# Optimization experiments

Measured on AMD Instinct MI355X. Metric: run time of the kernel, lower is better.

Reference implementation:

```python
import jax, jax.numpy as jnp
import numpy as np
import math

N_LAYER, N_EMBD, LAYER_ID = 12, 768, 0
B, T, C = 32, 1024, N_EMBD


def _init_params():
    r01 = LAYER_ID / (N_LAYER - 1)          # ratio_0_to_1
    r1a0 = 1.0 - LAYER_ID / N_LAYER          # ratio_1_to_almost0
    h = np.arange(C, dtype=np.float32)
    time_decay = (-5.0 + 8.0 * (h / (C - 1)) ** (0.7 + 1.3 * r01)).astype(np.float32)
    zigzag = (np.array([(i + 1) % 3 - 1 for i in range(C)], dtype=np.float32)) * 0.5
    time_first = (np.ones(C, dtype=np.float32) * math.log(0.3) + zigzag).astype(np.float32)
    xlin = (np.arange(C, dtype=np.float32) / C).reshape(1, 1, C)
    time_mix_k = np.power(xlin, r1a0).astype(np.float32)
    time_mix_v = (np.power(xlin, r1a0) + 0.3 * r01).astype(np.float32)
    time_mix_r = np.power(xlin, 0.5 * r1a0).astype(np.float32)
    return time_decay, time_first, time_mix_k, time_mix_v, time_mix_r


def setup_inputs() -> dict:
    key = jax.random.key(0)
    ks = jax.random.split(key, 5)
    td, tf, tmk, tmv, tmr = _init_params()
    scale = 0.02
    return {
        'x': jax.random.normal(ks[0], (B, T, C), dtype=jnp.float32),
        'time_decay': jnp.asarray(td),
        'time_first': jnp.asarray(tf),
        'time_mix_k': jnp.asarray(tmk),
        'time_mix_v': jnp.asarray(tmv),
        'time_mix_r': jnp.asarray(tmr),
        'Wk': jax.random.normal(ks[1], (C, C), dtype=jnp.float32) * scale,
        'Wv': jax.random.normal(ks[2], (C, C), dtype=jnp.float32) * scale,
        'Wr': jax.random.normal(ks[3], (C, C), dtype=jnp.float32) * scale,
        'Wo': jax.random.normal(ks[4], (C, C), dtype=jnp.float32) * scale,
    }


def _wkv(w, u, k, v):
    # Numerically-stable WKV recurrence (Vision-RWKV kernel math):
    # y_t = (sum_{i<t} exp(w*(t-1-i)+k_i) v_i + exp(u+k_t) v_t) / (same denom)
    # carry: p = num*exp(-o), q = den*exp(-o), o = running log-scale; shapes [B,C]
    def step(carry, kv):
        p, q, o = carry
        kt, vt = kv  # [B,C]
        no = jnp.maximum(o, u + kt)
        A = jnp.exp(o - no)
        Bc = jnp.exp(u + kt - no)
        y = (A * p + Bc * vt) / (A * q + Bc)
        no2 = jnp.maximum(w + o, kt)
        A2 = jnp.exp(w + o - no2)
        B2 = jnp.exp(kt - no2)
        return (A2 * p + B2 * vt, A2 * q + B2, no2), y

    b = k.shape[0]
    init = (jnp.zeros((b, C), jnp.float32), jnp.zeros((b, C), jnp.float32),
            jnp.full((b, C), -1e38, jnp.float32))
    kT = jnp.swapaxes(k, 0, 1)  # [T,B,C]
    vT = jnp.swapaxes(v, 0, 1)
    _, ys = jax.lax.scan(step, init, (kT, vT))
    return jnp.swapaxes(ys, 0, 1)  # [B,T,C]


def reference(x, time_decay, time_first, time_mix_k, time_mix_v, time_mix_r, Wk, Wv, Wr, Wo):
    # time_shift: xx[t] = x[t-1], xx[0] = 0
    xx = jnp.pad(x, ((0, 0), (1, 0), (0, 0)))[:, :-1, :]
    xk = x * time_mix_k + xx * (1.0 - time_mix_k)
    xv = x * time_mix_v + xx * (1.0 - time_mix_v)
    xr = x * time_mix_r + xx * (1.0 - time_mix_r)
    k = jnp.einsum('btc,oc->bto', xk, Wk)
    v = jnp.einsum('btc,oc->bto', xv, Wv)
    r = jnp.einsum('btc,oc->bto', xr, Wr)
    sr = jax.nn.sigmoid(r)
    y = _wkv(time_decay, time_first, k, v)
    return jnp.einsum('btc,oc->bto', sr * y, Wo)
```

## Files before the change

kernel.cpp:

```cpp
#include <hip/hip_runtime.h>
#include <math.h>

#define B_ 32
#define T_ 1024
#define C_ 768
#define M_ (B_ * T_)

typedef __attribute__((ext_vector_type(8))) short bf16x8;
typedef __attribute__((ext_vector_type(4))) float f32x4;
typedef __attribute__((ext_vector_type(8))) unsigned short u16x8;
typedef __attribute__((address_space(1))) const void g_void;
typedef __attribute__((address_space(3))) void lds_void;

__device__ __forceinline__ unsigned short f2bf(float f) {
  union { float f; unsigned int u; } v; v.f = f;
  unsigned int u = v.u;
  u += 0x7fffu + ((u >> 16) & 1u);
  return (unsigned short)(u >> 16);
}
__device__ __forceinline__ float b2f(unsigned short h) {
  union { unsigned int u; float f; } v; v.u = ((unsigned int)h) << 16;
  return v.f;
}
__device__ __forceinline__ float blo(unsigned int p) {
  union { unsigned int u; float f; } v; v.u = p << 16;
  return v.f;
}
__device__ __forceinline__ float bhi(unsigned int p) {
  union { unsigned int u; float f; } v; v.u = p & 0xffff0000u;
  return v.f;
}

#define WPB 288
#define WBLK (4 * WPB)
#define MBLK ((M_ * C_ / 8) / 256)

__global__ __launch_bounds__(256) void prep(const float* __restrict__ x,
                                            const float* __restrict__ tmk,
                                            const float* __restrict__ tmv,
                                            const float* __restrict__ tmr,
                                            const float* __restrict__ Wk,
                                            const float* __restrict__ Wv,
                                            const float* __restrict__ Wr,
                                            const float* __restrict__ Wo,
                                            unsigned short* __restrict__ wbk,
                                            unsigned short* __restrict__ wbv,
                                            unsigned short* __restrict__ wbr,
                                            unsigned short* __restrict__ wbo,
                                            unsigned short* __restrict__ ok,
                                            unsigned short* __restrict__ ov,
                                            unsigned short* __restrict__ orr) {
  if (blockIdx.x < WBLK) {
    const int sel = blockIdx.x / WPB;
    const int wi = blockIdx.x % WPB;
    const float* src = (sel == 0) ? Wk : (sel == 1) ? Wv : (sel == 2) ? Wr : Wo;
    unsigned short* dst = (sel == 0) ? wbk : (sel == 1) ? wbv : (sel == 2) ? wbr : wbo;
    const int gi = wi * 256 + threadIdx.x;
    const float* p = src + (size_t)gi * 8;
    float v[8];
    *(float4*)&v[0] = *(const float4*)p;
    *(float4*)&v[4] = *(const float4*)(p + 4);
    u16x8 o;
#pragma unroll
    for (int i = 0; i < 8; ++i) o[i] = f2bf(v[i]);
    *(u16x8*)(dst + (size_t)gi * 8) = o;
    return;
  }

  const unsigned int gi = (blockIdx.x - WBLK) * 256u + threadIdx.x;
  const int m = gi / (C_ / 8);
  const int c8 = (gi % (C_ / 8)) * 8;
  const float* xp = x + (size_t)m * C_ + c8;
  float xv8[8], xx8[8], t8[8];
  *(float4*)&xv8[0] = *(const float4*)xp;
  *(float4*)&xv8[4] = *(const float4*)(xp + 4);
  if ((m & (T_ - 1)) != 0) {
    *(float4*)&xx8[0] = *(const float4*)(xp - C_);
    *(float4*)&xx8[4] = *(const float4*)(xp - C_ + 4);
  } else {
#pragma unroll
    for (int i = 0; i < 8; ++i) xx8[i] = 0.f;
  }
  const size_t ob = (size_t)m * C_ + c8;

  *(float4*)&t8[0] = *(const float4*)(tmk + c8);
  *(float4*)&t8[4] = *(const float4*)(tmk + c8 + 4);
  u16x8 o;
#pragma unroll
  for (int i = 0; i < 8; ++i) o[i] = f2bf(xv8[i] * t8[i] + xx8[i] * (1.f - t8[i]));
  *(u16x8*)(ok + ob) = o;

  *(float4*)&t8[0] = *(const float4*)(tmv + c8);
  *(float4*)&t8[4] = *(const float4*)(tmv + c8 + 4);
#pragma unroll
  for (int i = 0; i < 8; ++i) o[i] = f2bf(xv8[i] * t8[i] + xx8[i] * (1.f - t8[i]));
  *(u16x8*)(ov + ob) = o;

  *(float4*)&t8[0] = *(const float4*)(tmr + c8);
  *(float4*)&t8[4] = *(const float4*)(tmr + c8 + 4);
#pragma unroll
  for (int i = 0; i < 8; ++i) o[i] = f2bf(xv8[i] * t8[i] + xx8[i] * (1.f - t8[i]));
  *(u16x8*)(orr + ob) = o;
}

#define GBM 128
#define GBN 128
#define GBK 64
#define GNB ((M_ / GBM) * (C_ / GBN))
#define NT (C_ / GBK)
#define BUFSZ 16384
#define BOFF_B 8192

#define WAITV(n) asm volatile("s_waitcnt vmcnt(" #n ")" ::: "memory")

template <int OUT_BF16>
__global__ __launch_bounds__(256) void gemm8(const unsigned short* __restrict__ A,
                                             const unsigned short* __restrict__ W,
                                             void* __restrict__ outv) {
  __shared__ unsigned short lds[2 * BUFSZ];

  int bid = (int)blockIdx.x;
  bid = (bid & 7) * (GNB / 8) + (bid >> 3);
  const int mt = bid / (C_ / GBN);
  const int nt = bid % (C_ / GBN);
  const int m0 = mt * GBM, n0 = nt * GBN;

  const int tid = threadIdx.x;
  const int lane = tid & 63;
  const int wv = tid >> 6;
  const int wm = wv >> 1;
  const int wn = wv & 1;

  const int l3 = lane >> 3;
  const int scol = (((lane & 7) ^ l3) << 3);
  const unsigned short* abase = A + (size_t)(m0 + wv * 8 + l3) * C_ + scol;
  const unsigned short* wbase = W + (size_t)(n0 + wv * 8 + l3) * C_ + scol;

#define STAGE(tt, bi)                                                         \
  {                                                                           \
    const int kk0_ = (tt) * GBK;                                              \
    _Pragma("unroll") for (int s_ = 0; s_ < 4; ++s_)                          \
        __builtin_amdgcn_global_load_lds(                                     \
            (g_void*)(abase + (size_t)s_ * 32 * C_ + kk0_),                   \
            (lds_void*)&lds[(bi) * BUFSZ + s_ * 2048 + wv * 512], 16, 0, 0);  \
    _Pragma("unroll") for (int s_ = 0; s_ < 4; ++s_)                          \
        __builtin_amdgcn_global_load_lds(                                     \
            (g_void*)(wbase + (size_t)s_ * 32 * C_ + kk0_),                   \
            (lds_void*)&lds[(bi) * BUFSZ + BOFF_B + s_ * 2048 + wv * 512],    \
            16, 0, 0);                                                        \
  }

  STAGE(0, 0);
  STAGE(1, 1);

  f32x4 acc[4][4] = {};
  const int arow = wm * 64 + (lane & 15);
  const int brow = wn * 64 + (lane & 15);

  for (int t = 0; t < NT; ++t) {
    if (t < NT - 1) { WAITV(8); }
    else { WAITV(0); }
    __builtin_amdgcn_s_barrier();
    __builtin_amdgcn_sched_barrier(0);

    const unsigned short* bufA = &lds[(t & 1) * BUFSZ];
    const unsigned short* bufB = bufA + BOFF_B;

#pragma unroll
    for (int kk = 0; kk < 2; ++kk) {
      const int sw = ((((kk << 2) | (lane >> 4)) ^ (lane & 7)) << 3);
      bf16x8 af[4], bfv[4];
#pragma unroll
      for (int f = 0; f < 4; ++f)
        af[f] = *(const bf16x8*)&bufA[(arow + f * 16) * 64 + sw];
#pragma unroll
      for (int f = 0; f < 4; ++f)
        bfv[f] = *(const bf16x8*)&bufB[(brow + f * 16) * 64 + sw];
      __builtin_amdgcn_s_setprio(1);
#pragma unroll
      for (int i = 0; i < 4; ++i)
#pragma unroll
        for (int j = 0; j < 4; ++j)
          acc[i][j] = __builtin_amdgcn_mfma_f32_16x16x32_bf16(af[i], bfv[j], acc[i][j], 0, 0, 0);
      __builtin_amdgcn_s_setprio(0);
    }

    __builtin_amdgcn_s_barrier();
    __builtin_amdgcn_sched_barrier(0);
    if (t + 2 < NT) STAGE(t + 2, t & 1);
  }

  const int crow0 = m0 + wm * 64 + (lane >> 4) * 4;
  const int ccol0 = n0 + wn * 64 + (lane & 15);
  if (OUT_BF16) {
    unsigned short* out = (unsigned short*)outv;
#pragma unroll
    for (int i = 0; i < 4; ++i)
#pragma unroll
      for (int j = 0; j < 4; ++j)
#pragma unroll
        for (int r = 0; r < 4; ++r)
          out[(size_t)(crow0 + i * 16 + r) * C_ + ccol0 + j * 16] = f2bf(acc[i][j][r]);
  } else {
    float* out = (float*)outv;
#pragma unroll
    for (int i = 0; i < 4; ++i)
#pragma unroll
      for (int j = 0; j < 4; ++j)
#pragma unroll
        for (int r = 0; r < 4; ++r)
          out[(size_t)(crow0 + i * 16 + r) * C_ + ccol0 + j * 16] = acc[i][j][r];
  }
#undef STAGE
}

#define NCH 32
#define CL  (T_ / NCH)

#define SCAN_STEP(w_, kt, vt, p_, q_, o_)                    \
  {                                                          \
    const float d_ = (w_ + o_) - (kt);                       \
    const float e_ = __expf(-fabsf(d_));                     \
    const float A_ = (d_ < 0.f) ? e_ : 1.f;                  \
    const float Bc_ = (d_ < 0.f) ? 1.f : e_;                 \
    p_ = A_ * p_ + Bc_ * (vt);                               \
    q_ = A_ * q_ + Bc_;                                      \
    o_ = fmaxf(w_ + o_, (kt));                               \
  }

#define KS_COMBINE(w_, lp_, lq_, lo_, p_, q_, o_, span_)     \
  {                                                          \
    const float dsp_ = (w_) * (float)(span_) + (lo_);        \
    const float dd_ = dsp_ - o_;                             \
    const float e_ = __expf(-fabsf(dd_));                    \
    const float ea_ = (dd_ < 0.f) ? e_ : 1.f;                \
    const float eb_ = (dd_ < 0.f) ? 1.f : e_;                \
    p_ = ea_ * (lp_) + eb_ * p_;                             \
    q_ = ea_ * (lq_) + eb_ * q_;                             \
    o_ = fmaxf(dsp_, o_);                                    \
  }

#define Y_STEP(w_, u_, kt, vt, rt, pp_, qq_, oo_, zres_)     \
  {                                                          \
    const float d1_ = oo_ - ((u_) + (kt));                   \
    const float e1_ = __expf(-fabsf(d1_));                   \
    const float Ae_ = (d1_ < 0.f) ? e1_ : 1.f;               \
    const float Be_ = (d1_ < 0.f) ? 1.f : e1_;               \
    const float er_ = __expf(-(rt));                         \
    zres_ = __fdividef(Ae_ * pp_ + Be_ * (vt),               \
                       (Ae_ * qq_ + Be_) * (1.f + er_));     \
    SCAN_STEP(w_, kt, vt, pp_, qq_, oo_)                     \
  }

__global__ __launch_bounds__(512) void wkv_scan(const unsigned short* __restrict__ kin,
                                                const unsigned short* __restrict__ vin,
                                                const unsigned short* __restrict__ rin,
                                                const float* __restrict__ wdec,
                                                const float* __restrict__ ufirst,
                                                unsigned short* __restrict__ z) {
  __shared__ float ps[NCH][64], qs[NCH][64], os[NCH][64];

  const int b = blockIdx.x / (C_ / 64);
  const int cg = blockIdx.x % (C_ / 64);
  const int ci = threadIdx.x & 31;
  const int j = threadIdx.x >> 5;
  const int jA = j, jB = j + 16;
  const int c0 = cg * 64 + 2 * ci;
  const float w0 = wdec[c0], w1 = wdec[c0 + 1];
  const float u0 = ufirst[c0], u1 = ufirst[c0 + 1];
  const size_t baseA = ((size_t)b * T_ + (size_t)jA * CL) * C_ + c0;
  const size_t baseB = ((size_t)b * T_ + (size_t)jB * CL) * C_ + c0;

  float Ap0 = 0.f, Aq0 = 0.f, Ao0 = -1e38f, Ap1 = 0.f, Aq1 = 0.f, Ao1 = -1e38f;
  float Bp0 = 0.f, Bq0 = 0.f, Bo0 = -1e38f, Bp1 = 0.f, Bq1 = 0.f, Bo1 = -1e38f;
  {
    size_t ia = baseA, ib = baseB;
#pragma unroll 4
    for (int t = 0; t < CL; ++t, ia += C_, ib += C_) {
      const unsigned int kA = *(const unsigned int*)(kin + ia);
      const unsigned int vA = *(const unsigned int*)(vin + ia);
      const unsigned int kB = *(const unsigned int*)(kin + ib);
      const unsigned int vB = *(const unsigned int*)(vin + ib);
      SCAN_STEP(w0, blo(kA), blo(vA), Ap0, Aq0, Ao0)
      SCAN_STEP(w1, bhi(kA), bhi(vA), Ap1, Aq1, Ao1)
      SCAN_STEP(w0, blo(kB), blo(vB), Bp0, Bq0, Bo0)
      SCAN_STEP(w1, bhi(kB), bhi(vB), Bp1, Bq1, Bo1)
    }
  }
  ps[jA][2 * ci] = Ap0; qs[jA][2 * ci] = Aq0; os[jA][2 * ci] = Ao0;
  ps[jA][2 * ci + 1] = Ap1; qs[jA][2 * ci + 1] = Aq1; os[jA][2 * ci + 1] = Ao1;
  ps[jB][2 * ci] = Bp0; qs[jB][2 * ci] = Bq0; os[jB][2 * ci] = Bo0;
  ps[jB][2 * ci + 1] = Bp1; qs[jB][2 * ci + 1] = Bq1; os[jB][2 * ci + 1] = Bo1;
  __syncthreads();

#pragma unroll
  for (int s = 1; s < NCH; s <<= 1) {
    float tAp0 = Ap0, tAq0 = Aq0, tAo0 = Ao0, tAp1 = Ap1, tAq1 = Aq1, tAo1 = Ao1;
    float tBp0 = Bp0, tBq0 = Bq0, tBo0 = Bo0, tBp1 = Bp1, tBq1 = Bq1, tBo1 = Bo1;
    if (jA >= s) {
      KS_COMBINE(w0, ps[jA - s][2 * ci], qs[jA - s][2 * ci], os[jA - s][2 * ci],
                 tAp0, tAq0, tAo0, s * CL)
      KS_COMBINE(w1, ps[jA - s][2 * ci + 1], qs[jA - s][2 * ci + 1], os[jA - s][2 * ci + 1],
                 tAp1, tAq1, tAo1, s * CL)
    }
    KS_COMBINE(w0, ps[jB - s][2 * ci], qs[jB - s][2 * ci], os[jB - s][2 * ci],
               tBp0, tBq0, tBo0, s * CL)
    KS_COMBINE(w1, ps[jB - s][2 * ci + 1], qs[jB - s][2 * ci + 1], os[jB - s][2 * ci + 1],
               tBp1, tBq1, tBo1, s * CL)
    __syncthreads();
    Ap0 = tAp0; Aq0 = tAq0; Ao0 = tAo0; Ap1 = tAp1; Aq1 = tAq1; Ao1 = tAo1;
    Bp0 = tBp0; Bq0 = tBq0; Bo0 = tBo0; Bp1 = tBp1; Bq1 = tBq1; Bo1 = tBo1;
    ps[jA][2 * ci] = Ap0; qs[jA][2 * ci] = Aq0; os[jA][2 * ci] = Ao0;
    ps[jA][2 * ci + 1] = Ap1; qs[jA][2 * ci + 1] = Aq1; os[jA][2 * ci + 1] = Ao1;
    ps[jB][2 * ci] = Bp0; qs[jB][2 * ci] = Bq0; os[jB][2 * ci] = Bo0;
    ps[jB][2 * ci + 1] = Bp1; qs[jB][2 * ci + 1] = Bq1; os[jB][2 * ci + 1] = Bo1;
    __syncthreads();
  }

  float pA0 = 0.f, qA0 = 0.f, oA0 = -1e38f, pA1 = 0.f, qA1 = 0.f, oA1 = -1e38f;
  if (j > 0) {
    pA0 = ps[jA - 1][2 * ci]; qA0 = qs[jA - 1][2 * ci]; oA0 = os[jA - 1][2 * ci];
    pA1 = ps[jA - 1][2 * ci + 1]; qA1 = qs[jA - 1][2 * ci + 1]; oA1 = os[jA - 1][2 * ci + 1];
  }
  float pB0 = ps[jB - 1][2 * ci], qB0 = qs[jB - 1][2 * ci], oB0 = os[jB - 1][2 * ci];
  float pB1 = ps[jB - 1][2 * ci + 1], qB1 = qs[jB - 1][2 * ci + 1], oB1 = os[jB - 1][2 * ci + 1];

  {
    size_t ia = baseA, ib = baseB;
#pragma unroll 4
    for (int t = 0; t < CL; ++t, ia += C_, ib += C_) {
      const unsigned int kA = *(const unsigned int*)(kin + ia);
      const unsigned int vA = *(const unsigned int*)(vin + ia);
      const unsigned int rA = *(const unsigned int*)(rin + ia);
      const unsigned int kB = *(const unsigned int*)(kin + ib);
      const unsigned int vB = *(const unsigned int*)(vin + ib);
      const unsigned int rB = *(const unsigned int*)(rin + ib);
      float y0, y1;
      Y_STEP(w0, u0, blo(kA), blo(vA), blo(rA), pA0, qA0, oA0, y0)
      Y_STEP(w1, u1, bhi(kA), bhi(vA), bhi(rA), pA1, qA1, oA1, y1)
      const unsigned int zoA = (unsigned int)f2bf(y0) | (((unsigned int)f2bf(y1)) << 16);
      Y_STEP(w0, u0, blo(kB), blo(vB), blo(rB), pB0, qB0, oB0, y0)
      Y_STEP(w1, u1, bhi(kB), bhi(vB), bhi(rB), pB1, qB1, oB1, y1)
      const unsigned int zoB = (unsigned int)f2bf(y0) | (((unsigned int)f2bf(y1)) << 16);
      *(unsigned int*)(z + ia) = zoA;
      *(unsigned int*)(z + ib) = zoB;
    }
  }
}

extern "C" void kernel_launch(void* const* d_in, const int* in_sizes, int n_in,
                              void* d_out, int out_size, void* d_ws,
                              size_t ws_size, hipStream_t stream) {
  const float* x   = (const float*)d_in[0];
  const float* td  = (const float*)d_in[1];
  const float* tf  = (const float*)d_in[2];
  const float* tmk = (const float*)d_in[3];
  const float* tmv = (const float*)d_in[4];
  const float* tmr = (const float*)d_in[5];
  const float* Wk  = (const float*)d_in[6];
  const float* Wv  = (const float*)d_in[7];
  const float* Wr  = (const float*)d_in[8];
  const float* Wo  = (const float*)d_in[9];

  const size_t nW = (size_t)C_ * C_;
  const size_t nM = (size_t)M_ * C_;

  unsigned short* wbk  = (unsigned short*)d_ws;
  unsigned short* wbv  = wbk + nW;
  unsigned short* wbr  = wbv + nW;
  unsigned short* wbo  = wbr + nW;
  unsigned short* xk   = wbo + nW;
  unsigned short* xv   = xk + nM;
  unsigned short* xr   = xv + nM;
  unsigned short* kbuf = xr + nM;
  unsigned short* vbuf = kbuf + nM;
  unsigned short* rbuf = (unsigned short*)d_out;
  unsigned short* zb   = xv;

  prep<<<WBLK + MBLK, 256, 0, stream>>>(x, tmk, tmv, tmr, Wk, Wv, Wr, Wo,
                                        wbk, wbv, wbr, wbo, xk, xv, xr);

  gemm8<1><<<GNB, 256, 0, stream>>>(xk, wbk, kbuf);
  gemm8<1><<<GNB, 256, 0, stream>>>(xv, wbv, vbuf);
  gemm8<1><<<GNB, 256, 0, stream>>>(xr, wbr, rbuf);

  wkv_scan<<<B_ * (C_ / 64), 512, 0, stream>>>(kbuf, vbuf, rbuf, td, tf, zb);

  gemm8<0><<<GNB, 256, 0, stream>>>(zb, wbo, d_out);
}
```

Baseline: 324.3 us.

## Fold time-mix into weights and fuse K/V/R projections into one GEMM

Folds the time-mix coefficients into the K, V and R weights, giving per-output [tm*W, (1-tm)*W] with K=1536. Prep now writes a single bf16 copy of x with a zero pad row per batch, so the shifted token is just the previous row. One GEMM with N=2304 then produces interleaved k/v/r, and the scan reads them at strided offsets. This removes the three mixed-activation buffers and two GEMM launches, at the cost of twice the matmul FLOPs for the projections.

```diff
diff --git a/kernel.cpp b/kernel.cpp
--- a/kernel.cpp
+++ b/kernel.cpp
@@ -5,6 +5,9 @@
 #define T_ 1024
 #define C_ 768
 #define M_ (B_ * T_)
+#define KN 2304
+#define KK 1536
+#define XROWS (B_ * (T_ + 1))
 
 typedef __attribute__((ext_vector_type(8))) short bf16x8;
 typedef __attribute__((ext_vector_type(4))) float f32x4;
@@ -18,10 +21,6 @@
   u += 0x7fffu + ((u >> 16) & 1u);
   return (unsigned short)(u >> 16);
 }
-__device__ __forceinline__ float b2f(unsigned short h) {
-  union { unsigned int u; float f; } v; v.u = ((unsigned int)h) << 16;
-  return v.f;
-}
 __device__ __forceinline__ float blo(unsigned int p) {
   union { unsigned int u; float f; } v; v.u = p << 16;
   return v.f;
@@ -31,92 +30,190 @@
   return v.f;
 }
 
-#define WPB 288
-#define WBLK (4 * WPB)
-#define MBLK ((M_ * C_ / 8) / 256)
-
-__global__ __launch_bounds__(256) void prep(const float* __restrict__ x,
-                                            const float* __restrict__ tmk,
-                                            const float* __restrict__ tmv,
-                                            const float* __restrict__ tmr,
-                                            const float* __restrict__ Wk,
-                                            const float* __restrict__ Wv,
-                                            const float* __restrict__ Wr,
-                                            const float* __restrict__ Wo,
-                                            unsigned short* __restrict__ wbk,
-                                            unsigned short* __restrict__ wbv,
-                                            unsigned short* __restrict__ wbr,
-                                            unsigned short* __restrict__ wbo,
-                                            unsigned short* __restrict__ ok,
-                                            unsigned short* __restrict__ ov,
-                                            unsigned short* __restrict__ orr) {
-  if (blockIdx.x < WBLK) {
-    const int sel = blockIdx.x / WPB;
-    const int wi = blockIdx.x % WPB;
-    const float* src = (sel == 0) ? Wk : (sel == 1) ? Wv : (sel == 2) ? Wr : Wo;
-    unsigned short* dst = (sel == 0) ? wbk : (sel == 1) ? wbv : (sel == 2) ? wbr : wbo;
+#define P_FOLD 864
+#define P_WO   1152
+#define P_X    13440
+#define P_END  13452
+
+__global__ __launch_bounds__(256) void prep2(const float* __restrict__ x,
+                                             const float* __restrict__ tmk,
+                                             const float* __restrict__ tmv,
+                                             const float* __restrict__ tmr,
+                                             const float* __restrict__ Wk,
+                                             const float* __restrict__ Wv,
+                                             const float* __restrict__ Wr,
+                                             const float* __restrict__ Wo,
+                                             unsigned short* __restrict__ Wp,
+                                             unsigned short* __restrict__ wbo,
+                                             unsigned short* __restrict__ xb) {
+  const int blk = blockIdx.x;
+  if (blk < P_FOLD) {
+    const int sel = blk / 288;
+    const int wi = blk % 288;
+    const float* W = (sel == 0) ? Wk : (sel == 1) ? Wv : Wr;
+    const float* tm = (sel == 0) ? tmk : (sel == 1) ? tmv : tmr;
     const int gi = wi * 256 + threadIdx.x;
-    const float* p = src + (size_t)gi * 8;
+    const int o = (gi * 8) / C_;
+    const int c0 = (gi * 8) % C_;
+    float wv8[8], t8[8];
+    *(float4*)&wv8[0] = *(const float4*)(W + (size_t)o * C_ + c0);
+    *(float4*)&wv8[4] = *(const float4*)(W + (size_t)o * C_ + c0 + 4);
+    *(float4*)&t8[0] = *(const float4*)(tm + c0);
+    *(float4*)&t8[4] = *(const float4*)(tm + c0 + 4);
+    u16x8 a, b;
+#pragma unroll
+    for (int i = 0; i < 8; ++i) {
+      a[i] = f2bf(t8[i] * wv8[i]);
+      b[i] = f2bf((1.f - t8[i]) * wv8[i]);
+    }
+    const size_t row = (size_t)(sel * C_ + o) * KK;
+    *(u16x8*)(Wp + row + c0) = a;
+    *(u16x8*)(Wp + row + C_ + c0) = b;
+    return;
+  }
+  if (blk < P_WO) {
+    const int gi = (blk - P_FOLD) * 256 + threadIdx.x;
+    const float* p = Wo + (size_t)gi * 8;
     float v[8];
     *(float4*)&v[0] = *(const float4*)p;
     *(float4*)&v[4] = *(const float4*)(p + 4);
     u16x8 o;
 #pragma unroll
     for (int i = 0; i < 8; ++i) o[i] = f2bf(v[i]);
-    *(u16x8*)(dst + (size_t)gi * 8) = o;
+    *(u16x8*)(wbo + (size_t)gi * 8) = o;
     return;
   }
-
-  const unsigned int gi = (blockIdx.x - WBLK) * 256u + threadIdx.x;
-  const int m = gi / (C_ / 8);
-  const int c8 = (gi % (C_ / 8)) * 8;
-  const float* xp = x + (size_t)m * C_ + c8;
-  float xv8[8], xx8[8], t8[8];
-  *(float4*)&xv8[0] = *(const float4*)xp;
-  *(float4*)&xv8[4] = *(const float4*)(xp + 4);
-  if ((m & (T_ - 1)) != 0) {
-    *(float4*)&xx8[0] = *(const float4*)(xp - C_);
-    *(float4*)&xx8[4] = *(const float4*)(xp - C_ + 4);
-  } else {
-#pragma unroll
-    for (int i = 0; i < 8; ++i) xx8[i] = 0.f;
-  }
-  const size_t ob = (size_t)m * C_ + c8;
-
-  *(float4*)&t8[0] = *(const float4*)(tmk + c8);
-  *(float4*)&t8[4] = *(const float4*)(tmk + c8 + 4);
-  u16x8 o;
-#pragma unroll
-  for (int i = 0; i < 8; ++i) o[i] = f2bf(xv8[i] * t8[i] + xx8[i] * (1.f - t8[i]));
-  *(u16x8*)(ok + ob) = o;
-
-  *(float4*)&t8[0] = *(const float4*)(tmv + c8);
-  *(float4*)&t8[4] = *(const float4*)(tmv + c8 + 4);
-#pragma unroll
-  for (int i = 0; i < 8; ++i) o[i] = f2bf(xv8[i] * t8[i] + xx8[i] * (1.f - t8[i]));
-  *(u16x8*)(ov + ob) = o;
-
-  *(float4*)&t8[0] = *(const float4*)(tmr + c8);
-  *(float4*)&t8[4] = *(const float4*)(tmr + c8 + 4);
-#pragma unroll
-  for (int i = 0; i < 8; ++i) o[i] = f2bf(xv8[i] * t8[i] + xx8[i] * (1.f - t8[i]));
-  *(u16x8*)(orr + ob) = o;
+  if (blk < P_X) {
+    const unsigned int gi = (blk - P_WO) * 256u + threadIdx.x;
+    const int m = gi / (C_ / 8);
+    const int c8 = (gi % (C_ / 8)) * 8;
+    const float* xp = x + (size_t)m * C_ + c8;
+    float v[8];
+    *(float4*)&v[0] = *(const float4*)xp;
+    *(float4*)&v[4] = *(const float4*)(xp + 4);
+    u16x8 o;
+#pragma unroll
+    for (int i = 0; i < 8; ++i) o[i] = f2bf(v[i]);
+    const int row = (m >> 10) * (T_ + 1) + (m & 1023) + 1;
+    *(u16x8*)(xb + (size_t)row * C_ + c8) = o;
+    return;
+  }
+  {
+    const int gi = (blk - P_X) * 256 + threadIdx.x;
+    const int b = gi / (C_ / 8);
+    const int c8 = (gi % (C_ / 8)) * 8;
+    u16x8 o = {};
+    *(u16x8*)(xb + (size_t)(b * (T_ + 1)) * C_ + c8) = o;
+  }
 }
 
 #define GBM 128
 #define GBN 128
 #define GBK 64
+#define BUFSZ 16384
+#define BOFF_B 8192
+#define WAITV(n) asm volatile("s_waitcnt vmcnt(" #n ")" ::: "memory")
+
+#define NT2 24
+#define GNB2 ((M_ / GBM) * (KN / GBN))
+
+__global__ __launch_bounds__(256) void gemm_kvr(const unsigned short* __restrict__ xb,
+                                                const unsigned short* __restrict__ Wp,
+                                                unsigned short* __restrict__ out) {
+  __shared__ unsigned short lds[2 * BUFSZ];
+
+  int bid = (int)blockIdx.x;
+  bid = (bid & 7) * (GNB2 / 8) + (bid >> 3);
+  const int mt = bid / (KN / GBN);
+  const int nt = bid % (KN / GBN);
+  const int m0 = mt * GBM, n0 = nt * GBN;
+
+  const int tid = threadIdx.x;
+  const int lane = tid & 63;
+  const int wv = tid >> 6;
+  const int wm = wv >> 1;
+  const int wn = wv & 1;
+
+  const int l3 = lane >> 3;
+  const int scol = (((lane & 7) ^ l3) << 3);
+  const int r1b = (m0 >> 10) * (T_ + 1) + (m0 & 1023) + 1;
+  const unsigned short* abase1 = xb + (size_t)(r1b + wv * 8 + l3) * C_ + scol;
+  const unsigned short* wbase = Wp + (size_t)(n0 + wv * 8 + l3) * KK + scol;
+
+#define STAGE(tt, bi)                                                         \
+  {                                                                           \
+    const unsigned short* asrc_ = ((tt) < 12)                                 \
+        ? (abase1 + (tt) * GBK)                                               \
+        : (abase1 - C_ + ((tt) - 12) * GBK);                                  \
+    _Pragma("unroll") for (int s_ = 0; s_ < 4; ++s_)                          \
+        __builtin_amdgcn_global_load_lds(                                     \
+            (g_void*)(asrc_ + (size_t)s_ * 32 * C_),                          \
+            (lds_void*)&lds[(bi) * BUFSZ + s_ * 2048 + wv * 512], 16, 0, 0);  \
+    _Pragma("unroll") for (int s_ = 0; s_ < 4; ++s_)                          \
+        __builtin_amdgcn_global_load_lds(                                     \
+            (g_void*)(wbase + (tt) * GBK + (size_t)s_ * 32 * KK),             \
+            (lds_void*)&lds[(bi) * BUFSZ + BOFF_B + s_ * 2048 + wv * 512],    \
+            16, 0, 0);                                                        \
+  }
+
+  STAGE(0, 0);
+  STAGE(1, 1);
+
+  f32x4 acc[4][4] = {};
+  const int arow = wm * 64 + (lane & 15);
+  const int brow = wn * 64 + (lane & 15);
+
+  for (int t = 0; t < NT2; ++t) {
+    if (t < NT2 - 1) { WAITV(8); }
+    else { WAITV(0); }
+    __builtin_amdgcn_s_barrier();
+    __builtin_amdgcn_sched_barrier(0);
+
+    const unsigned short* bufA = &lds[(t & 1) * BUFSZ];
+    const unsigned short* bufB = bufA + BOFF_B;
+
+#pragma unroll
+    for (int kk = 0; kk < 2; ++kk) {
+      const int sw = ((((kk << 2) | (lane >> 4)) ^ (lane & 7)) << 3);
+      bf16x8 af[4], bfv[4];
+#pragma unroll
+      for (int f = 0; f < 4; ++f)
+        af[f] = *(const bf16x8*)&bufA[(arow + f * 16) * 64 + sw];
+#pragma unroll
+      for (int f = 0; f < 4; ++f)
+        bfv[f] = *(const bf16x8*)&bufB[(brow + f * 16) * 64 + sw];
+      __builtin_amdgcn_s_setprio(1);
+#pragma unroll
+      for (int i = 0; i < 4; ++i)
+#pragma unroll
+        for (int j = 0; j < 4; ++j)
+          acc[i][j] = __builtin_amdgcn_mfma_f32_16x16x32_bf16(af[i], bfv[j], acc[i][j], 0, 0, 0);
+      __builtin_amdgcn_s_setprio(0);
+    }
+
+    __builtin_amdgcn_s_barrier();
+    __builtin_amdgcn_sched_barrier(0);
+    if (t + 2 < NT2) STAGE(t + 2, t & 1);
+  }
+
+  const int crow0 = m0 + wm * 64 + (lane >> 4) * 4;
+  const int ccol0 = n0 + wn * 64 + (lane & 15);
+#pragma unroll
+  for (int i = 0; i < 4; ++i)
+#pragma unroll
+    for (int j = 0; j < 4; ++j)
+#pragma unroll
+      for (int r = 0; r < 4; ++r)
+        out[(size_t)(crow0 + i * 16 + r) * KN + ccol0 + j * 16] = f2bf(acc[i][j][r]);
+#undef STAGE
+}
+
 #define GNB ((M_ / GBM) * (C_ / GBN))
 #define NT (C_ / GBK)
-#define BUFSZ 16384
-#define BOFF_B 8192
-
-#define WAITV(n) asm volatile("s_waitcnt vmcnt(" #n ")" ::: "memory")
-
-template <int OUT_BF16>
-__global__ __launch_bounds__(256) void gemm8(const unsigned short* __restrict__ A,
-                                             const unsigned short* __restrict__ W,
-                                             void* __restrict__ outv) {
+
+__global__ __launch_bounds__(256) void gemm_out(const unsigned short* __restrict__ A,
+                                                const unsigned short* __restrict__ W,
+                                                float* __restrict__ out) {
   __shared__ unsigned short lds[2 * BUFSZ];
 
   int bid = (int)blockIdx.x;
@@ -192,25 +289,13 @@
 
   const int crow0 = m0 + wm * 64 + (lane >> 4) * 4;
   const int ccol0 = n0 + wn * 64 + (lane & 15);
-  if (OUT_BF16) {
-    unsigned short* out = (unsigned short*)outv;
-#pragma unroll
-    for (int i = 0; i < 4; ++i)
-#pragma unroll
-      for (int j = 0; j < 4; ++j)
-#pragma unroll
-        for (int r = 0; r < 4; ++r)
-          out[(size_t)(crow0 + i * 16 + r) * C_ + ccol0 + j * 16] = f2bf(acc[i][j][r]);
-  } else {
-    float* out = (float*)outv;
-#pragma unroll
-    for (int i = 0; i < 4; ++i)
-#pragma unroll
-      for (int j = 0; j < 4; ++j)
-#pragma unroll
-        for (int r = 0; r < 4; ++r)
-          out[(size_t)(crow0 + i * 16 + r) * C_ + ccol0 + j * 16] = acc[i][j][r];
-  }
+#pragma unroll
+  for (int i = 0; i < 4; ++i)
+#pragma unroll
+    for (int j = 0; j < 4; ++j)
+#pragma unroll
+      for (int r = 0; r < 4; ++r)
+        out[(size_t)(crow0 + i * 16 + r) * C_ + ccol0 + j * 16] = acc[i][j][r];
 #undef STAGE
 }
 
@@ -252,9 +337,7 @@
     SCAN_STEP(w_, kt, vt, pp_, qq_, oo_)                     \
   }
 
-__global__ __launch_bounds__(512) void wkv_scan(const unsigned short* __restrict__ kin,
-                                                const unsigned short* __restrict__ vin,
-                                                const unsigned short* __restrict__ rin,
+__global__ __launch_bounds__(512) void wkv_scan(const unsigned short* __restrict__ kvr,
                                                 const float* __restrict__ wdec,
                                                 const float* __restrict__ ufirst,
                                                 unsigned short* __restrict__ z) {
@@ -268,19 +351,19 @@
   const int c0 = cg * 64 + 2 * ci;
   const float w0 = wdec[c0], w1 = wdec[c0 + 1];
   const float u0 = ufirst[c0], u1 = ufirst[c0 + 1];
-  const size_t baseA = ((size_t)b * T_ + (size_t)jA * CL) * C_ + c0;
-  const size_t baseB = ((size_t)b * T_ + (size_t)jB * CL) * C_ + c0;
+  const size_t rowA = (size_t)b * T_ + (size_t)jA * CL;
+  const size_t rowB = (size_t)b * T_ + (size_t)jB * CL;
 
   float Ap0 = 0.f, Aq0 = 0.f, Ao0 = -1e38f, Ap1 = 0.f, Aq1 = 0.f, Ao1 = -1e38f;
   float Bp0 = 0.f, Bq0 = 0.f, Bo0 = -1e38f, Bp1 = 0.f, Bq1 = 0.f, Bo1 = -1e38f;
   {
-    size_t ia = baseA, ib = baseB;
+    size_t ia = rowA * KN + c0, ib = rowB * KN + c0;
 #pragma unroll 4
-    for (int t = 0; t < CL; ++t, ia += C_, ib += C_) {
-      const unsigned int kA = *(const unsigned int*)(kin + ia);
-      const unsigned int vA = *(const unsigned int*)(vin + ia);
-      const unsigned int kB = *(const unsigned int*)(kin + ib);
-      const unsigned int vB = *(const unsigned int*)(vin + ib);
+    for (int t = 0; t < CL; ++t, ia += KN, ib += KN) {
+      const unsigned int kA = *(const unsigned int*)(kvr + ia);
+      const unsigned int vA = *(const unsigned int*)(kvr + ia + C_);
+      const unsigned int kB = *(const unsigned int*)(kvr + ib);
+      const unsigned int vB = *(const unsigned int*)(kvr + ib + C_);
       SCAN_STEP(w0, blo(kA), blo(vA), Ap0, Aq0, Ao0)
       SCAN_STEP(w1, bhi(kA), bhi(vA), Ap1, Aq1, Ao1)
       SCAN_STEP(w0, blo(kB), blo(vB), Bp0, Bq0, Bo0)
@@ -326,15 +409,16 @@
   float pB1 = ps[jB - 1][2 * ci + 1], qB1 = qs[jB - 1][2 * ci + 1], oB1 = os[jB - 1][2 * ci + 1];
 
   {
-    size_t ia = baseA, ib = baseB;
+    size_t ia = rowA * KN + c0, ib = rowB * KN + c0;
+    size_t za = rowA * C_ + c0, zbx = rowB * C_ + c0;
 #pragma unroll 4
-    for (int t = 0; t < CL; ++t, ia += C_, ib += C_) {
-      const unsigned int kA = *(const unsigned int*)(kin + ia);
-      const unsigned int vA = *(const unsigned int*)(vin + ia);
-      const unsigned int rA = *(const unsigned int*)(rin + ia);
-      const unsigned int kB = *(const unsigned int*)(kin + ib);
-      const unsigned int vB = *(const unsigned int*)(vin + ib);
-      const unsigned int rB = *(const unsigned int*)(rin + ib);
+    for (int t = 0; t < CL; ++t, ia += KN, ib += KN, za += C_, zbx += C_) {
+      const unsigned int kA = *(const unsigned int*)(kvr + ia);
+      const unsigned int vA = *(const unsigned int*)(kvr + ia + C_);
+      const unsigned int rA = *(const unsigned int*)(kvr + ia + 2 * C_);
+      const unsigned int kB = *(const unsigned int*)(kvr + ib);
+      const unsigned int vB = *(const unsigned int*)(kvr + ib + C_);
+      const unsigned int rB = *(const unsigned int*)(kvr + ib + 2 * C_);
       float y0, y1;
       Y_STEP(w0, u0, blo(kA), blo(vA), blo(rA), pA0, qA0, oA0, y0)
       Y_STEP(w1, u1, bhi(kA), bhi(vA), bhi(rA), pA1, qA1, oA1, y1)
@@ -342,8 +426,8 @@
       Y_STEP(w0, u0, blo(kB), blo(vB), blo(rB), pB0, qB0, oB0, y0)
       Y_STEP(w1, u1, bhi(kB), bhi(vB), bhi(rB), pB1, qB1, oB1, y1)
       const unsigned int zoB = (unsigned int)f2bf(y0) | (((unsigned int)f2bf(y1)) << 16);
-      *(unsigned int*)(z + ia) = zoA;
-      *(unsigned int*)(z + ib) = zoB;
+      *(unsigned int*)(z + za) = zoA;
+      *(unsigned int*)(z + zbx) = zoB;
     }
   }
 }
@@ -362,29 +446,17 @@
   const float* Wr  = (const float*)d_in[8];
   const float* Wo  = (const float*)d_in[9];
 
-  const size_t nW = (size_t)C_ * C_;
-  const size_t nM = (size_t)M_ * C_;
-
-  unsigned short* wbk  = (unsigned short*)d_ws;
-  unsigned short* wbv  = wbk + nW;
-  unsigned short* wbr  = wbv + nW;
-  unsigned short* wbo  = wbr + nW;
-  unsigned short* xk   = wbo + nW;
-  unsigned short* xv   = xk + nM;
-  unsigned short* xr   = xv + nM;
-  unsigned short* kbuf = xr + nM;
-  unsigned short* vbuf = kbuf + nM;
-  unsigned short* rbuf = (unsigned short*)d_out;
-  unsigned short* zb   = xv;
-
-  prep<<<WBLK + MBLK, 256, 0, stream>>>(x, tmk, tmv, tmr, Wk, Wv, Wr, Wo,
-                                        wbk, wbv, wbr, wbo, xk, xv, xr);
-
-  gemm8<1><<<GNB, 256, 0, stream>>>(xk, wbk, kbuf);
-  gemm8<1><<<GNB, 256, 0, stream>>>(xv, wbv, vbuf);
-  gemm8<1><<<GNB, 256, 0, stream>>>(xr, wbr, rbuf);
-
-  wkv_scan<<<B_ * (C_ / 64), 512, 0, stream>>>(kbuf, vbuf, rbuf, td, tf, zb);
-
-  gemm8<0><<<GNB, 256, 0, stream>>>(zb, wbo, d_out);
-}
+  unsigned short* Wp  = (unsigned short*)d_ws;
+  unsigned short* wbo = Wp + (size_t)KN * KK;
+  unsigned short* xb  = wbo + (size_t)C_ * C_;
+  unsigned short* kvr = xb + (size_t)XROWS * C_;
+  unsigned short* zb  = xb;
+
+  prep2<<<P_END, 256, 0, stream>>>(x, tmk, tmv, tmr, Wk, Wv, Wr, Wo, Wp, wbo, xb);
+
+  gemm_kvr<<<GNB2, 256, 0, stream>>>(xb, Wp, kvr);
+
+  wkv_scan<<<B_ * (C_ / 64), 512, 0, stream>>>(kvr, td, tf, zb);
+
+  gemm_out<<<GNB, 256, 0, stream>>>(zb, wbo, (float*)d_out);
+}
```

Measured after the change: 371.1 us. +14.5%, slower.
